# Kernel optimization log

Hardware: AMD Instinct MI355X
Metric: run time of the kernel (lower is better)

Reference implementation:

```python
import jax, jax.numpy as jnp
import numpy as np
from jax import lax

DN = ('NCHW', 'OIHW', 'NCHW')


def conv_reflect(x, w, b, pad):
    # reflect-padded Conv2d (padding_mode='reflect' in torch)
    xp = jnp.pad(x, ((0, 0), (0, 0), (pad, pad), (pad, pad)), mode='reflect')
    y = lax.conv_general_dilated(xp, w, (1, 1), 'VALID', dimension_numbers=DN)
    return y + b[None, :, None, None]


def setup_inputs() -> dict:
    key = jax.random.key(0)
    ks = jax.random.split(key, 11)
    B, C_in, W, H = 2, 20, 1024, 1024
    K = 16          # num_preconv_kernls
    P = 9           # preconv_kernel_size
    hid = 8         # hidden_input_size
    s = 0.05
    x = jax.random.normal(ks[0], (B, C_in, W, H), dtype=jnp.float32)
    w1 = jax.random.normal(ks[1], (16, 20, 7, 7), dtype=jnp.float32) * s
    b1 = jnp.zeros((16,), jnp.float32)
    w2 = jax.random.normal(ks[2], (32, 16, 5, 5), dtype=jnp.float32) * s
    b2 = jnp.zeros((32,), jnp.float32)
    w3 = jax.random.normal(ks[3], (64, 32, 5, 5), dtype=jnp.float32) * s
    b3 = jnp.zeros((64,), jnp.float32)
    w4 = jax.random.normal(ks[4], (hid + K, 64, 5, 5), dtype=jnp.float32) * s
    b4 = jnp.zeros((hid + K,), jnp.float32)
    dwk = (jnp.ones((K, 1, P, P), jnp.float32)
           + jax.random.normal(ks[5], (K, 1, P, P), dtype=jnp.float32) * 0.1) / (P * P)
    return {"x": x, "w1": w1, "b1": b1, "w2": w2, "b2": b2,
            "w3": w3, "b3": b3, "w4": w4, "b4": b4, "dwk": dwk}


def reference(x, w1, b1, w2, b2, w3, b3, w4, b4, dwk):
    B, _, W, H = x.shape
    hid, K, P = 8, 16, 9
    color = x[:, 0:3]                                   # (B,3,W,H)
    h = jax.nn.relu(conv_reflect(x, w1, b1, 3))
    h = jax.nn.relu(conv_reflect(h, w2, b2, 2))
    h = jax.nn.relu(conv_reflect(h, w3, b3, 2))
    raw = conv_reflect(h, w4, b4, 2)                    # (B,24,W,H)
    hidden = raw[:, 0:hid]                              # (B,8,W,H)
    weights = jax.nn.softmax(raw[:, hid:] / 5.0, axis=1)  # (B,16,W,H)
    # depthwise conv of color with 16 kernels per channel (groups=3, zero pad)
    rpk = jnp.tile(dwk, (3, 1, 1, 1))                   # (48,1,P,P)
    pre = lax.conv_general_dilated(color, rpk, (1, 1),
                                   [(P // 2, P // 2), (P // 2, P // 2)],
                                   dimension_numbers=DN,
                                   feature_group_count=3)
    pre = pre.reshape(B, 3, K, W, H)
    filtered = jnp.einsum('bkwh,bckwh->bcwh', weights, pre)
    return jnp.concatenate((filtered, hidden), axis=1)  # (B,11,W,H)
```

## Files before the change

kernel.cpp:

```cpp
#include <hip/hip_runtime.h>

constexpr int IMG = 1024;
constexpr long long HW = (long long)IMG * IMG;

typedef unsigned short u16;
typedef __attribute__((ext_vector_type(8))) short bf16x8;
typedef __attribute__((ext_vector_type(4))) float f32x4;
typedef __attribute__((ext_vector_type(4))) u16 u16x4;
typedef __attribute__((ext_vector_type(8))) u16 u16x8;

__device__ __forceinline__ int reflect_idx(int i, int n) {
    if (i < 0) i = -i;
    if (i >= n) i = 2 * n - 2 - i;
    return i;
}
__device__ __forceinline__ int iclamp(int v, int lo, int hi) {
    return v < lo ? lo : (v > hi ? hi : v);
}
__device__ __forceinline__ u16 f2bf(float f) {
    unsigned u = __builtin_bit_cast(unsigned, f);
    u += 0x7FFF + ((u >> 16) & 1);
    return (u16)(u >> 16);
}
__device__ __forceinline__ float bf2f(u16 v) {
    unsigned u = ((unsigned)v) << 16;
    return __builtin_bit_cast(float, u);
}

__global__ void prep_all(
    const float* __restrict__ w1, const float* __restrict__ w2,
    const float* __restrict__ w3, const float* __restrict__ w4,
    u16* __restrict__ w1p, u16* __restrict__ w2p,
    u16* __restrict__ w3p, u16* __restrict__ w4p)
{
    int i = blockIdx.x * 256 + threadIdx.x;
    if (i < 25088) {
        int tap = i / (16 * 32), rem = i % (16 * 32), co = rem / 32, ci = rem % 32;
        w1p[i] = (ci < 20) ? f2bf(w1[(co * 20 + ci) * 49 + tap]) : (u16)0;
        return;
    }
    i -= 25088;
    if (i < 13312) {
        int p = i / (32 * 32), rem = i % (32 * 32), co = rem / 32, k = rem % 32;
        int tap = 2 * p + (k >> 4), ci = k & 15;
        w2p[i] = (tap < 25) ? f2bf(w2[(co * 16 + ci) * 25 + tap]) : (u16)0;
        return;
    }
    i -= 13312;
    if (i < 51200) {
        int tap = i / (64 * 32), rem = i % (64 * 32), co = rem / 32, ci = rem % 32;
        w3p[i] = f2bf(w3[(co * 32 + ci) * 25 + tap]);
        return;
    }
    i -= 51200;
    if (i < 51200) {
        int tap = i / (32 * 64), rem = i % (32 * 64), co = rem / 64, ci = rem % 64;
        w4p[i] = (co < 24) ? f2bf(w4[(co * 64 + ci) * 25 + tap]) : (u16)0;
    }
}

__global__ __launch_bounds__(256) void conv1_mfma(
    const float* __restrict__ x, const u16* __restrict__ w1p,
    const float* __restrict__ b1, u16* __restrict__ h1, long long h1s,
    int out_base, int out_rows)
{
    constexpr int TS = 22, PAD = 3, UNITS = 4;
    __shared__ u16 tile[TS * TS * 32];

    const int tid = threadIdx.x;
    const int gx0 = blockIdx.x * 16;
    const int gy0 = out_base + blockIdx.y * 16;
    x  += (long long)blockIdx.z * 20 * HW;
    h1 += (long long)blockIdx.z * h1s;

    for (int u = tid; u < TS * TS * UNITS; u += 256) {
        int pu = u >> 2, q = u & 3;
        int ty = pu / TS, tx = pu - ty * TS;
        int gy = reflect_idx(gy0 + ty - PAD, IMG);
        int gx = reflect_idx(gx0 + tx - PAD, IMG);
        long long off = (long long)gy * IMG + gx;
        bf16x8 v;
        #pragma unroll
        for (int j = 0; j < 8; ++j) {
            int cc = q * 8 + j;
            float f = (cc < 20) ? x[(long long)cc * HW + off] : 0.f;
            v[j] = (short)f2bf(f);
        }
        *(bf16x8*)&tile[(pu * UNITS + (q ^ (tx & 3))) * 8] = v;
    }
    __syncthreads();

    const int lane = tid & 63, wv = tid >> 6;
    const int l15 = lane & 15, g = lane >> 4;

    f32x4 acc[4];
    #pragma unroll
    for (int y = 0; y < 4; ++y) acc[y] = (f32x4){0.f, 0.f, 0.f, 0.f};

    const u16* wp = w1p;
    for (int dx = 0; dx < 7; ++dx) {
        asm volatile("" : "+s"(wp));
        bf16x8 af[7];
        #pragma unroll
        for (int dy = 0; dy < 7; ++dy)
            af[dy] = *(const bf16x8*)&wp[((dy * 7 + dx) * 16 + l15) * 32 + g * 8];
        bf16x8 bfr[10];
        const int tx = l15 + dx;
        #pragma unroll
        for (int r = 0; r < 10; ++r)
            bfr[r] = *(const bf16x8*)&tile[(((wv * 4 + r) * TS + tx) * UNITS + (g ^ (tx & 3))) * 8];
        #pragma unroll
        for (int yy = 0; yy < 4; ++yy)
            #pragma unroll
            for (int dy = 0; dy < 7; ++dy)
                acc[yy] = __builtin_amdgcn_mfma_f32_16x16x32_bf16(af[dy], bfr[yy + dy], acc[yy], 0, 0, 0);
    }

    const int out_hi = out_base + out_rows;
    float bia[4];
    #pragma unroll
    for (int r = 0; r < 4; ++r) bia[r] = b1[4 * g + r];
    #pragma unroll
    for (int yy = 0; yy < 4; ++yy) {
        int gy = gy0 + wv * 4 + yy;
        if (gy >= out_hi) continue;
        u16x4 pk;
        #pragma unroll
        for (int r = 0; r < 4; ++r)
            pk[r] = f2bf(fmaxf(acc[yy][r] + bia[r], 0.f));
        *(u16x4*)&h1[((long long)(gy - out_base) * IMG + gx0 + l15) * 16 + 4 * g] = pk;
    }
}

__global__ __launch_bounds__(256) void conv2_mfma(
    const u16* __restrict__ h1, const u16* __restrict__ w2p,
    const float* __restrict__ b2, u16* __restrict__ h2,
    long long h1s, long long h2s,
    int in_base, int in_rows, int out_base, int out_rows)
{
    constexpr int TS = 20, PAD = 2, UNITS = 2;
    __shared__ u16 tile[TS * TS * 16];

    const int tid = threadIdx.x;
    const int gx0 = blockIdx.x * 16;
    const int gy0 = out_base + blockIdx.y * 16;
    h1 += (long long)blockIdx.z * h1s;
    h2 += (long long)blockIdx.z * h2s;

    for (int u = tid; u < TS * TS * UNITS; u += 256) {
        int pu = u >> 1, q = u & 1;
        int ty = pu / TS, tx = pu - ty * TS;
        int gy = reflect_idx(gy0 + ty - PAD, IMG) - in_base;
        gy = iclamp(gy, 0, in_rows - 1);
        int gx = reflect_idx(gx0 + tx - PAD, IMG);
        bf16x8 v = *(const bf16x8*)&h1[((long long)gy * IMG + gx) * 16 + q * 8];
        *(bf16x8*)&tile[(pu * UNITS + (q ^ (tx & 1))) * 8] = v;
    }
    __syncthreads();

    const int lane = tid & 63, wv = tid >> 6;
    const int l15 = lane & 15, g = lane >> 4;

    f32x4 acc[4][2];
    #pragma unroll
    for (int y = 0; y < 4; ++y) {
        acc[y][0] = (f32x4){0.f, 0.f, 0.f, 0.f};
        acc[y][1] = (f32x4){0.f, 0.f, 0.f, 0.f};
    }

    for (int p = 0; p < 13; ++p) {
        int tap = 2 * p + (g >> 1);
        int tb = tap > 24 ? 24 : tap;
        int dy = tb / 5, dx = tb - dy * 5;
        bf16x8 af0 = *(const bf16x8*)&w2p[(p * 32 + l15) * 32 + g * 8];
        bf16x8 af1 = *(const bf16x8*)&w2p[(p * 32 + 16 + l15) * 32 + g * 8];
        const int tx = l15 + dx;
        #pragma unroll
        for (int yy = 0; yy < 4; ++yy) {
            int ty = wv * 4 + yy + dy;
            bf16x8 bf = *(const bf16x8*)&tile[((ty * TS + tx) * UNITS + ((g & 1) ^ (tx & 1))) * 8];
            acc[yy][0] = __builtin_amdgcn_mfma_f32_16x16x32_bf16(af0, bf, acc[yy][0], 0, 0, 0);
            acc[yy][1] = __builtin_amdgcn_mfma_f32_16x16x32_bf16(af1, bf, acc[yy][1], 0, 0, 0);
        }
    }

    const int out_hi = out_base + out_rows;
    #pragma unroll
    for (int yy = 0; yy < 4; ++yy) {
        int gy = gy0 + wv * 4 + yy;
        if (gy >= out_hi) continue;
        long long pb = ((long long)(gy - out_base) * IMG + gx0 + l15) * 32;
        #pragma unroll
        for (int cb = 0; cb < 2; ++cb) {
            int co = cb * 16 + 4 * g;
            u16x4 pk;
            #pragma unroll
            for (int r = 0; r < 4; ++r)
                pk[r] = f2bf(fmaxf(acc[yy][cb][r] + b2[co + r], 0.f));
            *(u16x4*)&h2[pb + co] = pk;
        }
    }
}

__global__ __launch_bounds__(256) void conv3_mfma(
    const u16* __restrict__ h2, const u16* __restrict__ w3p,
    const float* __restrict__ b3, u16* __restrict__ h3,
    long long h2s, long long h3s,
    int in_base, int in_rows, int out_base, int out_rows)
{
    constexpr int CI = 32, TS = 20, PAD = 2, UNITS = 4;
    __shared__ u16 tileA[TS * TS * CI];
    __shared__ u16 tileB[TS * TS * CI];

    const int tid = threadIdx.x;
    const int gx0 = blockIdx.x * 16;
    const int gy0_0 = out_base + blockIdx.y * 64;
    const int lane = tid & 63, wv = tid >> 6;
    const int l15 = lane & 15, g = lane >> 4;
    const int out_hi = out_base + out_rows;
    h2 += (long long)blockIdx.z * h2s;
    h3 += (long long)blockIdx.z * h3s;

    auto STAGE = [&](u16* tl, int gy0) {
        for (int gidx = wv; gidx < 25; gidx += 4) {
            int j = (gidx << 6) + lane;
            int pu = j >> 2, qq = j & 3;
            int ty = pu / TS, tx = pu - ty * TS;
            int gy = iclamp(reflect_idx(gy0 + ty - PAD, IMG) - in_base, 0, in_rows - 1);
            int gx = reflect_idx(gx0 + tx - PAD, IMG);
            const u16* src = &h2[((long long)gy * IMG + gx) * CI + ((qq ^ (tx & 3)) << 3)];
            __builtin_amdgcn_global_load_lds(
                (const __attribute__((address_space(1))) void*)src,
                (__attribute__((address_space(3))) void*)&tl[(long long)gidx << 9],
                16, 0, 0);
        }
    };

    auto COMPUTE_EPI = [&](const u16* tl, int gy0) {
        f32x4 acc[4][4];
        #pragma unroll
        for (int y = 0; y < 4; ++y)
            #pragma unroll
            for (int cb = 0; cb < 4; ++cb) acc[y][cb] = (f32x4){0.f, 0.f, 0.f, 0.f};

        const u16* wp = w3p;
        for (int dx = 0; dx < 5; ++dx) {
            const int tx = l15 + dx;
            const int uu = g ^ (tx & 3);
            bf16x8 bfr[8];
            #pragma unroll
            for (int s = 0; s < 8; ++s)
                bfr[s] = *(const bf16x8*)&tl[(((wv * 4 + s) * TS + tx) * UNITS + uu) * 8];
            #pragma unroll
            for (int dy = 0; dy < 5; ++dy) {
                asm volatile("" : "+s"(wp));
                const int tap = dy * 5 + dx;
                bf16x8 af[4];
                #pragma unroll
                for (int cb = 0; cb < 4; ++cb)
                    af[cb] = *(const bf16x8*)&wp[(tap * 64 + cb * 16 + l15) * 32 + g * 8];
                #pragma unroll
                for (int yy = 0; yy < 4; ++yy)
                    #pragma unroll
                    for (int cb = 0; cb < 4; ++cb)
                        acc[yy][cb] = __builtin_amdgcn_mfma_f32_16x16x32_bf16(af[cb], bfr[yy + dy], acc[yy][cb], 0, 0, 0);
            }
        }

        #pragma unroll
        for (int yy = 0; yy < 4; ++yy) {
            int gy = gy0 + wv * 4 + yy;
            if (gy >= out_hi) continue;
            long long pb = ((long long)(gy - out_base) * IMG + gx0 + l15) * 64;
            #pragma unroll
            for (int cb = 0; cb < 4; ++cb) {
                int co = cb * 16 + 4 * g;
                u16x4 pk;
                #pragma unroll
                for (int r = 0; r < 4; ++r)
                    pk[r] = f2bf(fmaxf(acc[yy][cb][r] + b3[co + r], 0.f));
                *(u16x4*)&h3[pb + co] = pk;
            }
        }
    };

    STAGE(tileA, gy0_0);
    for (int t = 0; t < 4; ++t) {
        const int gy0 = gy0_0 + t * 16;
        if (gy0 >= out_hi) break;
        const u16* cur  = (t & 1) ? tileB : tileA;
        u16*       next = (t & 1) ? tileA : tileB;
        __syncthreads();
        if (t < 3) STAGE(next, gy0 + 16);
        COMPUTE_EPI(cur, gy0);
    }
}

__global__ __launch_bounds__(256) void conv4_mfma(
    const u16* __restrict__ h3, const u16* __restrict__ w4p,
    const float* __restrict__ b4, float* __restrict__ out,
    u16* __restrict__ wsoft, long long h3s, long long wss,
    int in_base, int in_rows, int row0, int nrows)
{
    constexpr int CI = 64, TSY = 20, TSX = 36, PAD = 2, UNITS = 4;
    __shared__ u16 tileA[TSY * TSX * 32];
    __shared__ u16 tileB[TSY * TSX * 32];

    const int tid = threadIdx.x;
    const int gx0 = blockIdx.x * 32;
    const int gy0_0 = row0 + blockIdx.y * 64;
    const int lane = tid & 63, wv = tid >> 6;
    const int l15 = lane & 15, g = lane >> 4;
    h3    += (long long)blockIdx.z * h3s;
    out   += (long long)blockIdx.z * 11 * HW;
    wsoft += (long long)blockIdx.z * wss;

    auto STAGE = [&](u16* tl, int gy0, int half) {
        for (int gidx = wv; gidx < 45; gidx += 4) {
            int j = (gidx << 6) + lane;
            int pu = j >> 2, qq = j & 3;
            int ty = pu / TSX, tx = pu - ty * TSX;
            int gy = iclamp(reflect_idx(gy0 + ty - PAD, IMG) - in_base, 0, in_rows - 1);
            int gx = reflect_idx(gx0 + tx - PAD, IMG);
            const u16* src = &h3[((long long)gy * IMG + gx) * CI + half * 32 + ((qq ^ (tx & 3)) << 3)];
            __builtin_amdgcn_global_load_lds(
                (const __attribute__((address_space(1))) void*)src,
                (__attribute__((address_space(3))) void*)&tl[(long long)gidx << 9],
                16, 0, 0);
        }
    };

    auto COMPUTE = [&](const u16* tl, int half, f32x4 (&acc)[4][2][2]) {
        for (int dx = 0; dx < 5; ++dx) {
            const int txL = l15 + dx;
            const int txR = txL + 16;
            const int uu = g ^ (txL & 3);
            bf16x8 bfL[8], bfR[8];
            #pragma unroll
            for (int s = 0; s < 8; ++s) {
                bfL[s] = *(const bf16x8*)&tl[(((wv * 4 + s) * TSX + txL) * UNITS + uu) * 8];
                bfR[s] = *(const bf16x8*)&tl[(((wv * 4 + s) * TSX + txR) * UNITS + uu) * 8];
            }
            #pragma unroll
            for (int dy = 0; dy < 5; ++dy) {
                const int tap = dy * 5 + dx;
                bf16x8 af0 = *(const bf16x8*)&w4p[(tap * 32 + l15) * 64 + half * 32 + g * 8];
                bf16x8 af1 = *(const bf16x8*)&w4p[(tap * 32 + 16 + l15) * 64 + half * 32 + g * 8];
                #pragma unroll
                for (int yy = 0; yy < 4; ++yy) {
                    acc[yy][0][0] = __builtin_amdgcn_mfma_f32_16x16x32_bf16(af0, bfL[yy + dy], acc[yy][0][0], 0, 0, 0);
                    acc[yy][1][0] = __builtin_amdgcn_mfma_f32_16x16x32_bf16(af1, bfL[yy + dy], acc[yy][1][0], 0, 0, 0);
                    acc[yy][0][1] = __builtin_amdgcn_mfma_f32_16x16x32_bf16(af0, bfR[yy + dy], acc[yy][0][1], 0, 0, 0);
                    acc[yy][1][1] = __builtin_amdgcn_mfma_f32_16x16x32_bf16(af1, bfR[yy + dy], acc[yy][1][1], 0, 0, 0);
                }
            }
        }
    };

    float bia0[4], bia1[4];
    #pragma unroll
    for (int r = 0; r < 4; ++r) {
        bia0[r] = b4[4 * g + r];
        int c1 = 16 + 4 * g + r;
        bia1[r] = (c1 < 24) ? b4[c1] : 0.f;
    }

    STAGE(tileA, gy0_0, 0);
    for (int t = 0; t < 4; ++t) {
        const int gy0 = gy0_0 + t * 16;
        f32x4 acc[4][2][2];
        #pragma unroll
        for (int y = 0; y < 4; ++y)
            #pragma unroll
            for (int cb = 0; cb < 2; ++cb) {
                acc[y][cb][0] = (f32x4){0.f, 0.f, 0.f, 0.f};
                acc[y][cb][1] = (f32x4){0.f, 0.f, 0.f, 0.f};
            }

        __syncthreads();
        STAGE(tileB, gy0, 1);
        COMPUTE(tileA, 0, acc);
        __syncthreads();
        if (t < 3) STAGE(tileA, gy0 + 16, 0);
        COMPUTE(tileB, 1, acc);

        #pragma unroll
        for (int ch = 0; ch < 2; ++ch) {
            const int col = gx0 + ch * 16 + l15;
            #pragma unroll
            for (int yy = 0; yy < 4; ++yy) {
                int gy = gy0 + wv * 4 + yy;
                long long pg = (long long)gy * IMG + col;
                float v0[4], v1[4];
                #pragma unroll
                for (int r = 0; r < 4; ++r) {
                    v0[r] = acc[yy][0][ch][r] + bia0[r];
                    v1[r] = acc[yy][1][ch][r] + bia1[r];
                }
                if (g < 2) {
                    #pragma unroll
                    for (int r = 0; r < 4; ++r)
                        out[(long long)(3 + 4 * g + r) * HW + pg] = v0[r];
                }
                float s[4];
                int kbase;
                if (g < 2) {
                    kbase = 8 + 4 * g;
                    #pragma unroll
                    for (int r = 0; r < 4; ++r) s[r] = v1[r] * 0.2f;
                } else {
                    kbase = 4 * (g - 2);
                    #pragma unroll
                    for (int r = 0; r < 4; ++r) s[r] = v0[r] * 0.2f;
                }
                float m = fmaxf(fmaxf(s[0], s[1]), fmaxf(s[2], s[3]));
                m = fmaxf(m, __shfl_xor(m, 16));
                m = fmaxf(m, __shfl_xor(m, 32));
                float e[4], loc = 0.f;
                #pragma unroll
                for (int r = 0; r < 4; ++r) { e[r] = __expf(s[r] - m); loc += e[r]; }
                loc += __shfl_xor(loc, 16);
                loc += __shfl_xor(loc, 32);
                float inv = 1.f / loc;
                long long pl = (long long)(gy - row0) * IMG + col;
                u16x4 pk;
                #pragma unroll
                for (int r = 0; r < 4; ++r) pk[r] = f2bf(e[r] * inv);
                *(u16x4*)&wsoft[pl * 16 + kbase] = pk;
            }
        }
    }
}

__global__ __launch_bounds__(256) void apply_filter(
    const float* __restrict__ x, const float* __restrict__ dwk,
    const u16* __restrict__ wsoft, float* __restrict__ out,
    long long wss, int row0, int nrows)
{
    constexpr int PAD = 4, TSF = 40;
    __shared__ float ctile[3][TSF * TSF];

    const int tid = threadIdx.x;
    const int tx = tid & 7, ty = tid >> 3;
    const int bx = blockIdx.x * 32;
    const int gy0 = row0 + blockIdx.y * 32;
    x     += (long long)blockIdx.z * 20 * HW;
    out   += (long long)blockIdx.z * 11 * HW;
    wsoft += (long long)blockIdx.z * wss;

    for (int c = 0; c < 3; ++c)
        for (int idx = tid; idx < TSF * TSF; idx += 256) {
            int ly = idx / TSF, lx = idx - ly * TSF;
            int gy = gy0 + ly - PAD, gx = bx + lx - PAD;
            float v = 0.f;
            if (gy >= 0 && gy < IMG && gx >= 0 && gx < IMG)
                v = x[(long long)c * HW + (long long)gy * IMG + gx];
            ctile[c][idx] = v;
        }
    __syncthreads();

    const int gy = gy0 + ty;
    const int xq = bx + tx * 4;

    float wreg[16][4];
    #pragma unroll
    for (int p = 0; p < 4; ++p) {
        long long pb = ((long long)(gy - row0) * IMG + xq + p) * 16;
        u16x8 lo = *(const u16x8*)&wsoft[pb];
        u16x8 hi = *(const u16x8*)&wsoft[pb + 8];
        #pragma unroll
        for (int k = 0; k < 8; ++k) {
            wreg[k][p]     = bf2f(lo[k]);
            wreg[8 + k][p] = bf2f(hi[k]);
        }
    }

    float f[3][4];
    #pragma unroll
    for (int c = 0; c < 3; ++c)
        #pragma unroll
        for (int p = 0; p < 4; ++p) f[c][p] = 0.f;

    for (int dy = 0; dy < 9; ++dy) {
        float c9[9][4];
        #pragma unroll
        for (int dxx = 0; dxx < 9; ++dxx)
            #pragma unroll
            for (int p = 0; p < 4; ++p) c9[dxx][p] = 0.f;
        #pragma unroll
        for (int k = 0; k < 16; ++k) {
            #pragma unroll
            for (int dxx = 0; dxx < 9; ++dxx) {
                float s = dwk[k * 81 + dy * 9 + dxx];
                #pragma unroll
                for (int p = 0; p < 4; ++p) c9[dxx][p] += s * wreg[k][p];
            }
        }
        #pragma unroll
        for (int c = 0; c < 3; ++c) {
            const float* crow = &ctile[c][(ty + dy) * TSF + tx * 4];
            f32x4 q0 = *(const f32x4*)crow;
            f32x4 q1 = *(const f32x4*)(crow + 4);
            f32x4 q2 = *(const f32x4*)(crow + 8);
            float win[12];
            #pragma unroll
            for (int j = 0; j < 4; ++j) { win[j] = q0[j]; win[4 + j] = q1[j]; win[8 + j] = q2[j]; }
            #pragma unroll
            for (int dxx = 0; dxx < 9; ++dxx)
                #pragma unroll
                for (int p = 0; p < 4; ++p)
                    f[c][p] += c9[dxx][p] * win[dxx + p];
        }
    }

    #pragma unroll
    for (int c = 0; c < 3; ++c) {
        f32x4 o = { f[c][0], f[c][1], f[c][2], f[c][3] };
        *(f32x4*)&out[(long long)c * HW + (long long)gy * IMG + xq] = o;
    }
}

static inline int hmax(int a, int b) { return a > b ? a : b; }
static inline int hmin(int a, int b) { return a < b ? a : b; }

extern "C" void kernel_launch(void* const* d_in, const int* in_sizes, int n_in,
                              void* d_out, int out_size, void* d_ws, size_t ws_size,
                              hipStream_t stream) {
    const float* x   = (const float*)d_in[0];
    const float* w1  = (const float*)d_in[1];
    const float* b1  = (const float*)d_in[2];
    const float* w2  = (const float*)d_in[3];
    const float* b2  = (const float*)d_in[4];
    const float* w3  = (const float*)d_in[5];
    const float* b3  = (const float*)d_in[6];
    const float* w4  = (const float*)d_in[7];
    const float* b4  = (const float*)d_in[8];
    const float* dwk = (const float*)d_in[9];
    float* out = (float*)d_out;

    int R = 64;
    const int cand[5] = {1024, 512, 256, 128, 64};
    for (int i = 0; i < 5; ++i) {
        long long r = cand[i];
        size_t per_batch = 32768ULL * (r + 12) + 65536ULL * (r + 8)
                         + 131072ULL * (r + 4) + 32768ULL * r;
        size_t need = 2 * per_batch + 400000ULL;
        if (need <= ws_size) { R = cand[i]; break; }
    }

    const long long h1s = (long long)(R + 12) * IMG * 16;
    const long long h2s = (long long)(R + 8) * IMG * 32;
    const long long h3s = (long long)(R + 4) * IMG * 64;
    const long long wss = (long long)R * IMG * 16;

    u16* h1    = (u16*)d_ws;
    u16* h2    = h1 + 2 * h1s;
    u16* h3    = h2 + 2 * h2s;
    u16* wsoft = h3 + 2 * h3s;
    u16* w1p   = wsoft + 2 * wss;
    u16* w2p   = w1p + 49 * 16 * 32;
    u16* w3p   = w2p + 13 * 32 * 32;
    u16* w4p   = w3p + 25 * 64 * 32;

    dim3 blk(256);
    prep_all<<<dim3(550), blk, 0, stream>>>(w1, w2, w3, w4, w1p, w2p, w3p, w4p);

    const int nstripes = IMG / R;
    for (int s = 0; s < nstripes; ++s) {
        const int r0 = s * R;
        const int h1_lo = hmax(0, r0 - 6), h1_hi = hmin(IMG, r0 + R + 6), h1_r = h1_hi - h1_lo;
        const int h2_lo = hmax(0, r0 - 4), h2_hi = hmin(IMG, r0 + R + 4), h2_r = h2_hi - h2_lo;
        const int h3_lo = hmax(0, r0 - 2), h3_hi = hmin(IMG, r0 + R + 2), h3_r = h3_hi - h3_lo;

        conv1_mfma<<<dim3(64, (h1_r + 15) / 16, 2), blk, 0, stream>>>(
            x, w1p, b1, h1, h1s, h1_lo, h1_r);
        conv2_mfma<<<dim3(64, (h2_r + 15) / 16, 2), blk, 0, stream>>>(
            h1, w2p, b2, h2, h1s, h2s, h1_lo, h1_r, h2_lo, h2_r);
        conv3_mfma<<<dim3(64, (h3_r + 63) / 64, 2), blk, 0, stream>>>(
            h2, w3p, b3, h3, h2s, h3s, h2_lo, h2_r, h3_lo, h3_r);
        conv4_mfma<<<dim3(32, R / 64, 2), blk, 0, stream>>>(
            h3, w4p, b4, out, wsoft, h3s, wss, h3_lo, h3_r, r0, R);
        apply_filter<<<dim3(32, R / 32, 2), blk, 0, stream>>>(
            x, dwk, wsoft, out, wss, r0, R);
    }
}
```

Baseline: 1.023 ms.

## Double-buffer conv2 tiles with async global-to-LDS loads over four row tiles

conv2 now processes four 16-row tiles per block instead of one. It stages the next halo tile into a second LDS buffer with global_load_lds while MFMAs run on the current one. The aim is to hide global-load latency behind compute and to amortize block setup. In exchange there are fewer blocks (less parallelism) and twice the LDS per block, which may lower occupancy.

After: 1.015 ms. Within noise of the previous version (-0.8%).

```diff
diff --git a/kernel.cpp b/kernel.cpp
--- a/kernel.cpp
+++ b/kernel.cpp
@@ -139,66 +139,86 @@
     int in_base, int in_rows, int out_base, int out_rows)
 {
     constexpr int TS = 20, PAD = 2, UNITS = 2;
-    __shared__ u16 tile[TS * TS * 16];
+    __shared__ u16 tileA[832 * 8];
+    __shared__ u16 tileB[832 * 8];
 
     const int tid = threadIdx.x;
     const int gx0 = blockIdx.x * 16;
-    const int gy0 = out_base + blockIdx.y * 16;
+    const int gy0_0 = out_base + blockIdx.y * 64;
+    const int lane = tid & 63, wv = tid >> 6;
+    const int l15 = lane & 15, g = lane >> 4;
+    const int out_hi = out_base + out_rows;
     h1 += (long long)blockIdx.z * h1s;
     h2 += (long long)blockIdx.z * h2s;
 
-    for (int u = tid; u < TS * TS * UNITS; u += 256) {
-        int pu = u >> 1, q = u & 1;
-        int ty = pu / TS, tx = pu - ty * TS;
-        int gy = reflect_idx(gy0 + ty - PAD, IMG) - in_base;
-        gy = iclamp(gy, 0, in_rows - 1);
-        int gx = reflect_idx(gx0 + tx - PAD, IMG);
-        bf16x8 v = *(const bf16x8*)&h1[((long long)gy * IMG + gx) * 16 + q * 8];
-        *(bf16x8*)&tile[(pu * UNITS + (q ^ (tx & 1))) * 8] = v;
-    }
-    __syncthreads();
-
-    const int lane = tid & 63, wv = tid >> 6;
-    const int l15 = lane & 15, g = lane >> 4;
-
-    f32x4 acc[4][2];
-    #pragma unroll
-    for (int y = 0; y < 4; ++y) {
-        acc[y][0] = (f32x4){0.f, 0.f, 0.f, 0.f};
-        acc[y][1] = (f32x4){0.f, 0.f, 0.f, 0.f};
-    }
-
-    for (int p = 0; p < 13; ++p) {
-        int tap = 2 * p + (g >> 1);
-        int tb = tap > 24 ? 24 : tap;
-        int dy = tb / 5, dx = tb - dy * 5;
-        bf16x8 af0 = *(const bf16x8*)&w2p[(p * 32 + l15) * 32 + g * 8];
-        bf16x8 af1 = *(const bf16x8*)&w2p[(p * 32 + 16 + l15) * 32 + g * 8];
-        const int tx = l15 + dx;
+    auto STAGE = [&](u16* tl, int gy0) {
+        for (int gidx = wv; gidx < 13; gidx += 4) {
+            int j = (gidx << 6) + lane;
+            int jc = j < 800 ? j : 799;
+            int pu = jc >> 1, qq = jc & 1;
+            int ty = pu / TS, tx = pu - ty * TS;
+            int gy = iclamp(reflect_idx(gy0 + ty - PAD, IMG) - in_base, 0, in_rows - 1);
+            int gx = reflect_idx(gx0 + tx - PAD, IMG);
+            const u16* src = &h1[((long long)gy * IMG + gx) * 16 + ((qq ^ (tx & 1)) << 3)];
+            __builtin_amdgcn_global_load_lds(
+                (const __attribute__((address_space(1))) void*)src,
+                (__attribute__((address_space(3))) void*)&tl[(long long)gidx << 9],
+                16, 0, 0);
+        }
+    };
+
+    auto COMPUTE_EPI = [&](const u16* tl, int gy0) {
+        f32x4 acc[4][2];
+        #pragma unroll
+        for (int y = 0; y < 4; ++y) {
+            acc[y][0] = (f32x4){0.f, 0.f, 0.f, 0.f};
+            acc[y][1] = (f32x4){0.f, 0.f, 0.f, 0.f};
+        }
+
+        const u16* wp = w2p;
+        for (int p = 0; p < 13; ++p) {
+            asm volatile("" : "+s"(wp));
+            int tap = 2 * p + (g >> 1);
+            int tb = tap > 24 ? 24 : tap;
+            int dy = tb / 5, dx = tb - dy * 5;
+            bf16x8 af0 = *(const bf16x8*)&wp[(p * 32 + l15) * 32 + g * 8];
+            bf16x8 af1 = *(const bf16x8*)&wp[(p * 32 + 16 + l15) * 32 + g * 8];
+            const int tx = l15 + dx;
+            #pragma unroll
+            for (int yy = 0; yy < 4; ++yy) {
+                int ty = wv * 4 + yy + dy;
+                bf16x8 bf = *(const bf16x8*)&tl[((ty * TS + tx) * UNITS + ((g & 1) ^ (tx & 1))) * 8];
+                acc[yy][0] = __builtin_amdgcn_mfma_f32_16x16x32_bf16(af0, bf, acc[yy][0], 0, 0, 0);
+                acc[yy][1] = __builtin_amdgcn_mfma_f32_16x16x32_bf16(af1, bf, acc[yy][1], 0, 0, 0);
+            }
+        }
+
         #pragma unroll
         for (int yy = 0; yy < 4; ++yy) {
-            int ty = wv * 4 + yy + dy;
-            bf16x8 bf = *(const bf16x8*)&tile[((ty * TS + tx) * UNITS + ((g & 1) ^ (tx & 1))) * 8];
-            acc[yy][0] = __builtin_amdgcn_mfma_f32_16x16x32_bf16(af0, bf, acc[yy][0], 0, 0, 0);
-            acc[yy][1] = __builtin_amdgcn_mfma_f32_16x16x32_bf16(af1, bf, acc[yy][1], 0, 0, 0);
-        }
-    }
-
-    const int out_hi = out_base + out_rows;
-    #pragma unroll
-    for (int yy = 0; yy < 4; ++yy) {
-        int gy = gy0 + wv * 4 + yy;
-        if (gy >= out_hi) continue;
-        long long pb = ((long long)(gy - out_base) * IMG + gx0 + l15) * 32;
-        #pragma unroll
-        for (int cb = 0; cb < 2; ++cb) {
-            int co = cb * 16 + 4 * g;
-            u16x4 pk;
-            #pragma unroll
-            for (int r = 0; r < 4; ++r)
-                pk[r] = f2bf(fmaxf(acc[yy][cb][r] + b2[co + r], 0.f));
-            *(u16x4*)&h2[pb + co] = pk;
-        }
+            int gy = gy0 + wv * 4 + yy;
+            if (gy >= out_hi) continue;
+            long long pb = ((long long)(gy - out_base) * IMG + gx0 + l15) * 32;
+            #pragma unroll
+            for (int cb = 0; cb < 2; ++cb) {
+                int co = cb * 16 + 4 * g;
+                u16x4 pk;
+                #pragma unroll
+                for (int r = 0; r < 4; ++r)
+                    pk[r] = f2bf(fmaxf(acc[yy][cb][r] + b2[co + r], 0.f));
+                *(u16x4*)&h2[pb + co] = pk;
+            }
+        }
+    };
+
+    STAGE(tileA, gy0_0);
+    for (int t = 0; t < 4; ++t) {
+        const int gy0 = gy0_0 + t * 16;
+        if (gy0 >= out_hi) break;
+        const u16* cur  = (t & 1) ? tileB : tileA;
+        u16*       next = (t & 1) ? tileA : tileB;
+        __syncthreads();
+        if (t < 3) STAGE(next, gy0 + 16);
+        COMPUTE_EPI(cur, gy0);
     }
 }
 
@@ -574,7 +594,7 @@
 
         conv1_mfma<<<dim3(64, (h1_r + 15) / 16, 2), blk, 0, stream>>>(
             x, w1p, b1, h1, h1s, h1_lo, h1_r);
-        conv2_mfma<<<dim3(64, (h2_r + 15) / 16, 2), blk, 0, stream>>>(
+        conv2_mfma<<<dim3(64, (h2_r + 63) / 64, 2), blk, 0, stream>>>(
             h1, w2p, b2, h2, h1s, h2s, h1_lo, h1_r, h2_lo, h2_r);
         conv3_mfma<<<dim3(64, (h3_r + 63) / 64, 2), blk, 0, stream>>>(
             h2, w3p, b3, h3, h2s, h3s, h2_lo, h2_r, h3_lo, h3_r);
```
